# Kernel tuning notes

Hardware: AMD Instinct MI355X
Metric: run time of the kernel (lower is better)

The kernel has to match this reference:

```python
import jax, jax.numpy as jnp
import numpy as np

TEMP = 0.1
LAM = 1.0
NORM_EPS = 1e-12   # torch F.normalize eps
COS_EPS = 1e-8     # torch F.cosine_similarity eps


def l2norm(x, axis):
    n = jnp.sqrt(jnp.sum(x * x, axis=axis, keepdims=True))
    return x / jnp.maximum(n, NORM_EPS)


def cos_sim(a, b, axis):
    na = jnp.sqrt(jnp.sum(a * a, axis=axis))
    nb = jnp.sqrt(jnp.sum(b * b, axis=axis))
    return jnp.sum(a * b, axis=axis) / jnp.maximum(na * nb, COS_EPS)


def setup_inputs() -> dict:
    key = jax.random.key(0)
    k1, k2, k3, k4, k5 = jax.random.split(key, 5)
    B, C, H, W = 32, 256, 32, 32
    return {
        "q_b": jax.random.normal(k1, (B, C, H, W), dtype=jnp.float32),
        "k_b": jax.random.normal(k2, (B, C, H, W), dtype=jnp.float32),
        "q_grid": jax.random.normal(k3, (B, C, H, W), dtype=jnp.float32),
        "k_grid": jax.random.normal(k4, (B, C, H, W), dtype=jnp.float32),
        "labels": jax.random.randint(k5, (B,), 0, 10, dtype=jnp.int64),
    }


def densecl(q_b, k_b, q_grid, k_grid, labels):
    B, C, H, W = q_b.shape
    S = H * W
    q_b = l2norm(q_b, axis=1)
    k_b = l2norm(k_b, axis=1)
    q_grid = l2norm(q_grid, axis=1)
    k_grid = l2norm(k_grid, axis=1)

    q_b_flat = q_b.reshape(B, C, S)
    k_b_flat = k_b.reshape(B, C, S)
    # spatial correspondence: [B, S, S]
    sim = jnp.einsum('bci,bcj->bij', q_b_flat, k_b_flat)
    max_sim_idx = jnp.argmax(sim, axis=-1)  # [B, S]

    Cg = q_grid.shape[1]
    q_grid_flat = q_grid.reshape(B, Cg, S)
    k_grid_flat = k_grid.reshape(B, Cg, S)
    idx = jnp.broadcast_to(max_sim_idx[:, None, :], (B, Cg, S))
    k_matched = jnp.take_along_axis(k_grid_flat, idx, axis=2)
    pos_sim = cos_sim(q_grid_flat, k_matched, axis=1) / TEMP  # [B, S]

    # random negative from a different-label sample (use_prototypes=False path)
    key = jax.random.key(42)
    u = jax.random.uniform(key, (B, B))
    mask = labels[:, None] != labels[None, :]
    neg_idx = jnp.argmax(jnp.where(mask, u, -1.0), axis=1)  # [B]
    neg_k = k_grid_flat[neg_idx]  # [B, Cg, S]
    neg_sim = cos_sim(q_grid_flat, neg_k, axis=1) / TEMP  # [B, S]

    loss = -jnp.log(jnp.exp(pos_sim) / (jnp.exp(pos_sim) + jnp.exp(neg_sim) + 1e-6))
    return jnp.mean(loss)


def reference(q_b, k_b, q_grid, k_grid, labels):
    return densecl(q_b, k_b, q_grid, k_grid, labels) * LAM
```

## Files before the change

kernel.cpp:

```cpp
#include <hip/hip_runtime.h>
#include <hip/hip_bf16.h>
#include <math.h>
#include <stdint.h>

#define BB 32
#define CC 256
#define SS 1024

typedef __attribute__((ext_vector_type(8))) short short8v;
typedef __attribute__((ext_vector_type(4))) float f32x4;

#define ASYNC16(g, l)                                                        \
  __builtin_amdgcn_global_load_lds(                                          \
      (const __attribute__((address_space(1))) void*)(g),                    \
      (__attribute__((address_space(3))) void*)(l), 16, 0, 0)

__device__ __forceinline__ unsigned short bf16_rne(float f) {
  unsigned int u = __float_as_uint(f);
  unsigned int r = (u + 0x7fffu + ((u >> 16) & 1u)) >> 16;
  return (unsigned short)r;
}

__device__ __forceinline__ void tf_round(uint32_t& x0, uint32_t& x1, int r) {
  x0 += x1;
  x1 = (x1 << r) | (x1 >> (32 - r));
  x1 ^= x0;
}

__device__ __forceinline__ void tf_gen(int t, float* u) {
  uint32_t x0 = (uint32_t)t;
  uint32_t x1 = (uint32_t)(t + 512);
  const uint32_t ks0 = 0u, ks1 = 42u, ks2 = 0x1BD11BDAu ^ 0u ^ 42u;
  x0 += ks0; x1 += ks1;
  tf_round(x0, x1, 13); tf_round(x0, x1, 15); tf_round(x0, x1, 26); tf_round(x0, x1, 6);
  x0 += ks1; x1 += ks2 + 1u;
  tf_round(x0, x1, 17); tf_round(x0, x1, 29); tf_round(x0, x1, 16); tf_round(x0, x1, 24);
  x0 += ks2; x1 += ks0 + 2u;
  tf_round(x0, x1, 13); tf_round(x0, x1, 15); tf_round(x0, x1, 26); tf_round(x0, x1, 6);
  x0 += ks0; x1 += ks1 + 3u;
  tf_round(x0, x1, 17); tf_round(x0, x1, 29); tf_round(x0, x1, 16); tf_round(x0, x1, 24);
  x0 += ks1; x1 += ks2 + 4u;
  tf_round(x0, x1, 13); tf_round(x0, x1, 15); tf_round(x0, x1, 26); tf_round(x0, x1, 6);
  x0 += ks2; x1 += ks0 + 5u;
  u[t]       = __uint_as_float((x0 >> 9) | 0x3f800000u) - 1.0f;
  u[t + 512] = __uint_as_float((x1 >> 9) | 0x3f800000u) - 1.0f;
}

__global__ __launch_bounds__(256, 4) void transnorm_kernel(
    const float* __restrict__ qb, const float* __restrict__ kb,
    const float* __restrict__ kg, unsigned short* __restrict__ qt,
    unsigned short* __restrict__ kt, unsigned short* __restrict__ kgt,
    float* __restrict__ invqb, float* __restrict__ invkb,
    float* __restrict__ invkg, const int* __restrict__ labels,
    int* __restrict__ negidx, unsigned long long* __restrict__ best,
    float* __restrict__ out) {
  const int bid = blockIdx.x;
  const int tid = threadIdx.x;

  __shared__ unsigned int tile[64 * 128];
  __shared__ float part[16][65];

  if (bid >= 1536) {
    if (bid == 1536) {
      float* u = (float*)&tile[0];
      tf_gen(tid, u);
      tf_gen(tid + 256, u);
      if (tid == 0) *out = 0.f;
      __syncthreads();
      if (tid < BB) {
        int lb = labels[tid];
        float bestv = -1.0f;
        int bj = 0;
        for (int j = 0; j < BB; ++j) {
          float v = (labels[j] != lb) ? u[tid * BB + j] : -1.0f;
          if (v > bestv) { bestv = v; bj = j; }
        }
        negidx[tid] = bj;
      }
    } else {
      unsigned long long* bp = best + (size_t)(bid - 1537) * 8192 + tid;
#pragma unroll
      for (int i = 0; i < 32; ++i) bp[(size_t)i * 256] = 0ull;
    }
    return;
  }

  const int which = bid >> 9;
  const int sub = bid & 511;
  const int b = sub >> 4;
  const int s0 = (sub & 15) * 64;

  const float* src = (which == 0) ? qb : (which == 1) ? kb : kg;
  unsigned short* dst = (which == 0) ? qt : (which == 1) ? kt : kgt;
  float* inv = (which == 0) ? invqb : (which == 1) ? invkb : invkg;

  const int sg = tid & 15;
  const int cq = tid >> 4;

  const float* sp = src + (size_t)b * CC * SS + s0 + sg * 4;
  float ssq[4] = {0.f, 0.f, 0.f, 0.f};

#pragma unroll
  for (int half = 0; half < 2; ++half) {
    float4 xa[4], xb[4];
#pragma unroll
    for (int kk = 0; kk < 4; ++kk) {
      int cp = cq + 16 * (half * 4 + kk);
      int c = cp * 2;
      xa[kk] = *(const float4*)(sp + ((size_t)c << 10));
      xb[kk] = *(const float4*)(sp + ((size_t)(c + 1) << 10));
    }
#pragma unroll
    for (int kk = 0; kk < 4; ++kk) {
      int cp = cq + 16 * (half * 4 + kk);
      float a[4] = {xa[kk].x, xa[kk].y, xa[kk].z, xa[kk].w};
      float bb[4] = {xb[kk].x, xb[kk].y, xb[kk].z, xb[kk].w};
#pragma unroll
      for (int e = 0; e < 4; ++e) {
        ssq[e] = fmaf(a[e], a[e], ssq[e]);
        ssq[e] = fmaf(bb[e], bb[e], ssq[e]);
        int r = sg * 4 + e;
        int colp = cp ^ (sg << 2);
        tile[r * 128 + colp] =
            (unsigned)bf16_rne(a[e]) | ((unsigned)bf16_rne(bb[e]) << 16);
      }
    }
  }
#pragma unroll
  for (int e = 0; e < 4; ++e) part[cq][sg * 4 + e] = ssq[e];
  __syncthreads();

  const int h = tid >> 5, cw = tid & 31;
  unsigned short* dp = dst + ((size_t)b * SS + s0) * CC;
#pragma unroll
  for (int p = 0; p < 8; ++p) {
    int r = p * 8 + h;
    int colb = (cw * 4) ^ ((r >> 2) << 2);
    uint4 pk = *(const uint4*)&tile[r * 128 + colb];
    *(uint4*)(dp + (size_t)r * CC + cw * 8) = pk;
  }
  if (tid < 64) {
    float s = 0.f;
#pragma unroll
    for (int k = 0; k < 16; ++k) s += part[k][tid];
    inv[b * SS + s0 + tid] = 1.0f / fmaxf(sqrtf(s), 1e-12f);
  }
}

__global__ __launch_bounds__(256, 3) void simargmax_mfma(
    const unsigned short* __restrict__ qt, const unsigned short* __restrict__ kt,
    const float* __restrict__ invk, unsigned long long* __restrict__ best) {
  const int bid0 = blockIdx.x;
  const int W = (bid0 & 7) * 256 + (bid0 >> 3);
  const int b = W >> 6, it = (W >> 3) & 7, jt = W & 7;
  const int t = threadIdx.x, w = t >> 6, l = t & 63;

  __shared__ unsigned short sa[128 * 64];
  __shared__ unsigned short sb[128 * 64];
  __shared__ unsigned long long cand2[128][2];
  __shared__ float sinvk[128];

  if (t < 128) sinvk[t] = invk[b * SS + jt * 128 + t];

  const unsigned short* aG = qt + ((size_t)b * SS + it * 128) * CC;
  const unsigned short* bG = kt + ((size_t)b * SS + jt * 128) * CC;

  f32x4 acc[4][4];
#pragma unroll
  for (int mt = 0; mt < 4; ++mt)
#pragma unroll
    for (int nt = 0; nt < 4; ++nt) acc[mt][nt] = (f32x4){0.f, 0.f, 0.f, 0.f};

  const int r8 = l >> 3, p = l & 7;
  const int q4 = l >> 4, m16 = l & 15;
  const int wi = (w >> 1) * 64, wj = (w & 1) * 64;

  for (int ch = 0; ch < 4; ++ch) {
    __syncthreads();
#pragma unroll
    for (int v = 0; v < 4; ++v) {
      int r = v * 32 + w * 8 + r8;
      int clog = p ^ (r & 7);
      ASYNC16(aG + (size_t)r * CC + ch * 64 + clog * 8, &sa[(v * 32 + w * 8) * 64]);
      ASYNC16(bG + (size_t)r * CC + ch * 64 + clog * 8, &sb[(v * 32 + w * 8) * 64]);
    }
    __syncthreads();
#pragma unroll
    for (int kk = 0; kk < 2; ++kk) {
      short8v af[4], bf[4];
#pragma unroll
      for (int mt = 0; mt < 4; ++mt) {
        int i = wi + mt * 16 + m16;
        int cp = (kk * 4 + q4) ^ (i & 7);
        af[mt] = *(const short8v*)&sa[i * 64 + cp * 8];
        int j = wj + mt * 16 + m16;
        int cq = (kk * 4 + q4) ^ (j & 7);
        bf[mt] = *(const short8v*)&sb[j * 64 + cq * 8];
      }
#pragma unroll
      for (int mt = 0; mt < 4; ++mt)
#pragma unroll
        for (int nt = 0; nt < 4; ++nt)
          acc[mt][nt] = __builtin_amdgcn_mfma_f32_16x16x32_bf16(
              af[mt], bf[nt], acc[mt][nt], 0, 0, 0);
    }
  }

  float siv[4];
#pragma unroll
  for (int nt = 0; nt < 4; ++nt) siv[nt] = sinvk[wj + nt * 16 + m16];

  unsigned long long bp[4][4];
#pragma unroll
  for (int mt = 0; mt < 4; ++mt) {
#pragma unroll
    for (int e = 0; e < 4; ++e) {
      unsigned long long mx = 0ull;
#pragma unroll
      for (int nt = 0; nt < 4; ++nt) {
        float v = acc[mt][nt][e] * siv[nt];
        unsigned int u = __float_as_uint(v);
        u = (u & 0x80000000u) ? ~u : (u | 0x80000000u);
        int col = jt * 128 + wj + nt * 16 + m16;
        unsigned long long pk =
            ((unsigned long long)u << 32) | (unsigned)(1023 - col);
        mx = (pk > mx) ? pk : mx;
      }
      bp[mt][e] = mx;
    }
  }
#pragma unroll
  for (int d = 1; d < 16; d <<= 1) {
#pragma unroll
    for (int mt = 0; mt < 4; ++mt)
#pragma unroll
      for (int e = 0; e < 4; ++e) {
        unsigned long long o = __shfl_xor(bp[mt][e], d, 64);
        if (o > bp[mt][e]) bp[mt][e] = o;
      }
  }
  if (m16 == 0) {
#pragma unroll
    for (int mt = 0; mt < 4; ++mt)
#pragma unroll
      for (int e = 0; e < 4; ++e)
        cand2[wi + mt * 16 + q4 * 4 + e][w & 1] = bp[mt][e];
  }
  __syncthreads();
  if (t < 128) {
    unsigned long long m0 = cand2[t][0], m1 = cand2[t][1];
    atomicMax(&best[b * SS + it * 128 + t], m0 > m1 ? m0 : m1);
  }
}

__global__ void negidx_kernel(const int* __restrict__ labels, int* __restrict__ negidx) {
  __shared__ float u[1024];
  int t = threadIdx.x;
  tf_gen(t, u);
  __syncthreads();
  if (t < BB) {
    int lb = labels[t];
    float bestv = -1.0f;
    int bj = 0;
    for (int j = 0; j < BB; ++j) {
      float v = (labels[j] != lb) ? u[t * BB + j] : -1.0f;
      if (v > bestv) { bestv = v; bj = j; }
    }
    negidx[t] = bj;
  }
}

__global__ __launch_bounds__(256) void loss_fused_kernel(
    const float* __restrict__ qg, const unsigned short* __restrict__ kgt,
    const float* __restrict__ invkg, const unsigned long long* __restrict__ best,
    const int* __restrict__ negidx, float* __restrict__ out) {
  const int tid = threadIdx.x;
  const int s_l = tid & 31, g = tid >> 5;
  const int P0 = blockIdx.x * 32;
  const int b = P0 >> 10;
  const int s = (P0 & (SS - 1)) + s_l;
  const int idx = b * SS + s;
  const int js = 1023 - (int)(best[idx] & 0xffffffffu);
  const int nb = negidx[b];

  const float* qcol = qg + ((size_t)b * CC + g * 32) * SS + s;
  const unsigned short* kp = kgt + ((size_t)b * SS + js) * CC + g * 32;
  const unsigned short* kn = kgt + ((size_t)nb * SS + s) * CC + g * 32;

  float dp = 0.f, dn = 0.f, sq = 0.f;
#pragma unroll
  for (int uu = 0; uu < 4; ++uu) {
    uint4 up = *(const uint4*)(kp + uu * 8);
    uint4 un = *(const uint4*)(kn + uu * 8);
    float q[8];
#pragma unroll
    for (int j = 0; j < 8; ++j) {
      q[j] = qcol[(size_t)(uu * 8 + j) << 10];
      sq = fmaf(q[j], q[j], sq);
    }
    float pv[8], nv[8];
    pv[0] = __uint_as_float(up.x << 16); pv[1] = __uint_as_float(up.x & 0xffff0000u);
    pv[2] = __uint_as_float(up.y << 16); pv[3] = __uint_as_float(up.y & 0xffff0000u);
    pv[4] = __uint_as_float(up.z << 16); pv[5] = __uint_as_float(up.z & 0xffff0000u);
    pv[6] = __uint_as_float(up.w << 16); pv[7] = __uint_as_float(up.w & 0xffff0000u);
    nv[0] = __uint_as_float(un.x << 16); nv[1] = __uint_as_float(un.x & 0xffff0000u);
    nv[2] = __uint_as_float(un.y << 16); nv[3] = __uint_as_float(un.y & 0xffff0000u);
    nv[4] = __uint_as_float(un.z << 16); nv[5] = __uint_as_float(un.z & 0xffff0000u);
    nv[6] = __uint_as_float(un.w << 16); nv[7] = __uint_as_float(un.w & 0xffff0000u);
#pragma unroll
    for (int j = 0; j < 8; ++j) {
      dp = fmaf(q[j], pv[j], dp);
      dn = fmaf(q[j], nv[j], dn);
    }
  }

  __shared__ float rdp[8][33], rdn[8][33], rsq[8][33];
  rdp[g][s_l] = dp;
  rdn[g][s_l] = dn;
  rsq[g][s_l] = sq;
  __syncthreads();
  if (tid < 32) {
    float DP = 0.f, DN = 0.f, SQ = 0.f;
#pragma unroll
    for (int k = 0; k < 8; ++k) {
      DP += rdp[k][tid];
      DN += rdn[k][tid];
      SQ += rsq[k][tid];
    }
    int s2 = (P0 & (SS - 1)) + tid;
    int idx2 = b * SS + s2;
    int js2 = 1023 - (int)(best[idx2] & 0xffffffffu);
    float iq = 1.0f / fmaxf(sqrtf(SQ), 1e-12f);
    float pvv = DP * iq * invkg[b * SS + js2] * 10.0f;
    float nvv = DN * iq * invkg[nb * SS + s2] * 10.0f;
    float elem = logf(expf(pvv) + expf(nvv) + 1e-6f) - pvv;
#pragma unroll
    for (int o = 16; o > 0; o >>= 1) elem += __shfl_down(elem, o, 32);
    if (tid == 0) atomicAdd(out, elem * (1.0f / (BB * SS)));
  }
}

__global__ __launch_bounds__(256) void norms_kernel(
    const float* __restrict__ qb, const float* __restrict__ kb,
    const float* __restrict__ qg, const float* __restrict__ kg,
    float* __restrict__ inv) {
  int t = blockIdx.x * 256 + threadIdx.x;
  int which = t >> 15;
  int bs = t & (BB * SS - 1);
  const float* src = (which == 0) ? qb : (which == 1) ? kb : (which == 2) ? qg : kg;
  int b = bs >> 10;
  int s = bs & (SS - 1);
  const float* p = src + (size_t)b * CC * SS + s;
  float ss = 0.f;
#pragma unroll 8
  for (int c = 0; c < CC; ++c) {
    float x = p[(size_t)c * SS];
    ss = fmaf(x, x, ss);
  }
  float n = fmaxf(sqrtf(ss), 1e-12f);
  inv[t] = 1.0f / n;
}

#define TI 64
#define TJ 128
#define KC 32

__global__ __launch_bounds__(256) void simargmax_kernel(
    const float* __restrict__ qb, const float* __restrict__ kb,
    const float* __restrict__ invq, const float* __restrict__ invk,
    int* __restrict__ amax) {
  const int b = blockIdx.x >> 4;
  const int i0 = (blockIdx.x & 15) * TI;
  const int t = threadIdx.x;
  const int ti = t >> 4;
  const int tj = t & 15;

  __shared__ float aQ[KC][TI];
  __shared__ float bK[KC][TJ];
  __shared__ float redv[TI][16];
  __shared__ int redj[TI][16];

  const float* qbase = qb + (size_t)b * CC * SS + i0;
  const float* kbase = kb + (size_t)b * CC * SS;
  const float* ivq = invq + b * SS + i0;
  const float* ivk = invk + b * SS;

  float best_v = -3.4e38f;
  int best_j = 0;

  for (int j0 = 0; j0 < SS; j0 += TJ) {
    float acc[4][8];
#pragma unroll
    for (int r = 0; r < 4; ++r)
#pragma unroll
      for (int rr = 0; rr < 8; ++rr) acc[r][rr] = 0.f;

    for (int c0 = 0; c0 < CC; c0 += KC) {
      __syncthreads();
#pragma unroll
      for (int v = 0; v < 2; ++v) {
        int f = t + v * 256;
        int cl = f >> 4;
        int sl = (f & 15) << 2;
        float4 qa = *(const float4*)(qbase + (size_t)(c0 + cl) * SS + sl);
        float4 iv = *(const float4*)(ivq + sl);
        aQ[cl][sl + 0] = qa.x * iv.x;
        aQ[cl][sl + 1] = qa.y * iv.y;
        aQ[cl][sl + 2] = qa.z * iv.z;
        aQ[cl][sl + 3] = qa.w * iv.w;
      }
#pragma unroll
      for (int v = 0; v < 4; ++v) {
        int f = t + v * 256;
        int cl = f >> 5;
        int sl = (f & 31) << 2;
        float4 ka = *(const float4*)(kbase + (size_t)(c0 + cl) * SS + j0 + sl);
        float4 ik = *(const float4*)(ivk + j0 + sl);
        bK[cl][sl + 0] = ka.x * ik.x;
        bK[cl][sl + 1] = ka.y * ik.y;
        bK[cl][sl + 2] = ka.z * ik.z;
        bK[cl][sl + 3] = ka.w * ik.w;
      }
      __syncthreads();
#pragma unroll
      for (int kc = 0; kc < KC; ++kc) {
        float4 a0 = *(const float4*)&aQ[kc][ti * 4];
        float4 b0 = *(const float4*)&bK[kc][tj * 8];
        float4 b1 = *(const float4*)&bK[kc][tj * 8 + 4];
        float av[4] = {a0.x, a0.y, a0.z, a0.w};
        float bv[8] = {b0.x, b0.y, b0.z, b0.w, b1.x, b1.y, b1.z, b1.w};
#pragma unroll
        for (int r = 0; r < 4; ++r)
#pragma unroll
          for (int rr = 0; rr < 8; ++rr)
            acc[r][rr] = fmaf(av[r], bv[rr], acc[r][rr]);
      }
    }
    __syncthreads();
#pragma unroll
    for (int r = 0; r < 4; ++r) {
      float v = acc[r][0];
      int jb = j0 + tj * 8;
#pragma unroll
      for (int rr = 1; rr < 8; ++rr) {
        if (acc[r][rr] > v) { v = acc[r][rr]; jb = j0 + tj * 8 + rr; }
      }
      redv[ti * 4 + r][tj] = v;
      redj[ti * 4 + r][tj] = jb;
    }
    __syncthreads();
    if (t < TI) {
#pragma unroll
      for (int ww = 0; ww < 16; ++ww) {
        float v = redv[t][ww];
        if (v > best_v) { best_v = v; best_j = redj[t][ww]; }
      }
    }
  }
  if (t < TI) amax[b * SS + i0 + t] = best_j;
}

__global__ __launch_bounds__(256) void loss_kernel(
    const float* __restrict__ qg, const float* __restrict__ kg,
    const float* __restrict__ invq, const float* __restrict__ invk,
    const int* __restrict__ amax, const int* __restrict__ negidx,
    float* __restrict__ out) {
  int t = blockIdx.x * 256 + threadIdx.x;
  int b = t >> 10;
  int s = t & (SS - 1);
  int js = amax[t];
  int nb = negidx[b];
  const float* qcol = qg + (size_t)b * CC * SS + s;
  const float* kpcol = kg + (size_t)b * CC * SS + js;
  const float* kncol = kg + (size_t)nb * CC * SS + s;
  float dp = 0.f, dn = 0.f;
#pragma unroll 8
  for (int c = 0; c < CC; ++c) {
    float q = qcol[(size_t)c * SS];
    dp = fmaf(q, kpcol[(size_t)c * SS], dp);
    dn = fmaf(q, kncol[(size_t)c * SS], dn);
  }
  float iq = invq[t];
  float pv = dp * iq * invk[b * SS + js] * 10.0f;
  float nv = dn * iq * invk[nb * SS + s] * 10.0f;
  float elem = logf(expf(pv) + expf(nv) + 1e-6f) - pv;

  __shared__ float red[256];
  red[threadIdx.x] = elem;
  __syncthreads();
  for (int o = 128; o > 0; o >>= 1) {
    if (threadIdx.x < o) red[threadIdx.x] += red[threadIdx.x + o];
    __syncthreads();
  }
  if (threadIdx.x == 0) atomicAdd(out, red[0] * (1.0f / (BB * SS)));
}

extern "C" void kernel_launch(void* const* d_in, const int* in_sizes, int n_in,
                              void* d_out, int out_size, void* d_ws, size_t ws_size,
                              hipStream_t stream) {
  const float* qb = (const float*)d_in[0];
  const float* kb = (const float*)d_in[1];
  const float* qg = (const float*)d_in[2];
  const float* kg = (const float*)d_in[3];
  const int* labels = (const int*)d_in[4];

  char* ws = (char*)d_ws;
  float* invqb = (float*)ws;
  float* invkb = (float*)(ws + 128 * 1024);
  float* invkg = (float*)(ws + 256 * 1024);
  unsigned long long* best = (unsigned long long*)(ws + 384 * 1024);
  int* negidx = (int*)(ws + 640 * 1024);
  unsigned short* qt = (unsigned short*)(ws + (1 << 20));
  unsigned short* kt = (unsigned short*)(ws + (17 << 20));
  unsigned short* kgt = (unsigned short*)(ws + (33 << 20));

  const size_t need = (size_t)49 * 1024 * 1024;
  const bool fast = ws_size >= need;

  if (fast) {
    transnorm_kernel<<<1541, 256, 0, stream>>>(qb, kb, kg, qt, kt, kgt, invqb,
                                               invkb, invkg, labels, negidx,
                                               best, (float*)d_out);
    simargmax_mfma<<<2048, 256, 0, stream>>>(qt, kt, invkb, best);
    loss_fused_kernel<<<1024, 256, 0, stream>>>(qg, kgt, invkg, best, negidx,
                                                (float*)d_out);
  } else {
    hipMemsetAsync(d_out, 0, sizeof(float), stream);
    float* inv = (float*)ws;
    int* amax = (int*)(ws + 512 * 1024);
    int* negidx2 = (int*)(ws + 640 * 1024);
    norms_kernel<<<(4 * BB * SS) / 256, 256, 0, stream>>>(qb, kb, qg, kg, inv);
    simargmax_kernel<<<BB * (SS / TI), 256, 0, stream>>>(
        qb, kb, inv + 0 * BB * SS, inv + 1 * BB * SS, amax);
    negidx_kernel<<<1, 512, 0, stream>>>(labels, negidx2);
    loss_kernel<<<(BB * SS) / 256, 256, 0, stream>>>(
        qg, kg, inv + 2 * BB * SS, inv + 3 * BB * SS, amax, negidx2,
        (float*)d_out);
  }
}
```

Measured before the change: 204.7 us.

## Double-buffer LDS tiles in similarity argmax kernel to overlap loads with MFMA

Splits the shared-memory A/B tiles of the similarity/argmax MFMA kernel into two buffers. The async global-to-LDS load of the next K chunk is issued before the MFMA compute on the current chunk, so fetch latency can be hidden behind compute instead of sitting between two barriers. The larger LDS footprint led to lowering the launch-bounds occupancy hint from 3 to 2 blocks per CU, which trades some latency hiding across blocks for this intra-block overlap. The K loop is now fully unrolled into four explicit stages.

```diff
diff --git a/kernel.cpp b/kernel.cpp
--- a/kernel.cpp
+++ b/kernel.cpp
@@ -147,7 +147,43 @@
   }
 }
 
-__global__ __launch_bounds__(256, 3) void simargmax_mfma(
+__device__ __forceinline__ void sim_stage(
+    const unsigned short* __restrict__ aG, const unsigned short* __restrict__ bG,
+    unsigned short* SA, unsigned short* SB, int ch, int w, int r8, int p) {
+#pragma unroll
+  for (int v = 0; v < 4; ++v) {
+    int r = v * 32 + w * 8 + r8;
+    int clog = p ^ (r & 7);
+    ASYNC16(aG + (size_t)r * CC + ch * 64 + clog * 8, &SA[(v * 32 + w * 8) * 64]);
+    ASYNC16(bG + (size_t)r * CC + ch * 64 + clog * 8, &SB[(v * 32 + w * 8) * 64]);
+  }
+}
+
+__device__ __forceinline__ void sim_compute(
+    const unsigned short* SA, const unsigned short* SB, f32x4 acc[4][4],
+    int wi, int wj, int q4, int m16) {
+#pragma unroll
+  for (int kk = 0; kk < 2; ++kk) {
+    short8v af[4], bf[4];
+#pragma unroll
+    for (int mt = 0; mt < 4; ++mt) {
+      int i = wi + mt * 16 + m16;
+      int cp = (kk * 4 + q4) ^ (i & 7);
+      af[mt] = *(const short8v*)&SA[i * 64 + cp * 8];
+      int j = wj + mt * 16 + m16;
+      int cq = (kk * 4 + q4) ^ (j & 7);
+      bf[mt] = *(const short8v*)&SB[j * 64 + cq * 8];
+    }
+#pragma unroll
+    for (int mt = 0; mt < 4; ++mt)
+#pragma unroll
+      for (int nt = 0; nt < 4; ++nt)
+        acc[mt][nt] = __builtin_amdgcn_mfma_f32_16x16x32_bf16(
+            af[mt], bf[nt], acc[mt][nt], 0, 0, 0);
+  }
+}
+
+__global__ __launch_bounds__(256, 2) void simargmax_mfma(
     const unsigned short* __restrict__ qt, const unsigned short* __restrict__ kt,
     const float* __restrict__ invk, unsigned long long* __restrict__ best) {
   const int bid0 = blockIdx.x;
@@ -155,8 +191,10 @@
   const int b = W >> 6, it = (W >> 3) & 7, jt = W & 7;
   const int t = threadIdx.x, w = t >> 6, l = t & 63;
 
-  __shared__ unsigned short sa[128 * 64];
-  __shared__ unsigned short sb[128 * 64];
+  __shared__ unsigned short sa0[128 * 64];
+  __shared__ unsigned short sa1[128 * 64];
+  __shared__ unsigned short sb0[128 * 64];
+  __shared__ unsigned short sb1[128 * 64];
   __shared__ unsigned long long cand2[128][2];
   __shared__ float sinvk[128];
 
@@ -175,36 +213,18 @@
   const int q4 = l >> 4, m16 = l & 15;
   const int wi = (w >> 1) * 64, wj = (w & 1) * 64;
 
-  for (int ch = 0; ch < 4; ++ch) {
-    __syncthreads();
-#pragma unroll
-    for (int v = 0; v < 4; ++v) {
-      int r = v * 32 + w * 8 + r8;
-      int clog = p ^ (r & 7);
-      ASYNC16(aG + (size_t)r * CC + ch * 64 + clog * 8, &sa[(v * 32 + w * 8) * 64]);
-      ASYNC16(bG + (size_t)r * CC + ch * 64 + clog * 8, &sb[(v * 32 + w * 8) * 64]);
-    }
-    __syncthreads();
-#pragma unroll
-    for (int kk = 0; kk < 2; ++kk) {
-      short8v af[4], bf[4];
-#pragma unroll
-      for (int mt = 0; mt < 4; ++mt) {
-        int i = wi + mt * 16 + m16;
-        int cp = (kk * 4 + q4) ^ (i & 7);
-        af[mt] = *(const short8v*)&sa[i * 64 + cp * 8];
-        int j = wj + mt * 16 + m16;
-        int cq = (kk * 4 + q4) ^ (j & 7);
-        bf[mt] = *(const short8v*)&sb[j * 64 + cq * 8];
-      }
-#pragma unroll
-      for (int mt = 0; mt < 4; ++mt)
-#pragma unroll
-        for (int nt = 0; nt < 4; ++nt)
-          acc[mt][nt] = __builtin_amdgcn_mfma_f32_16x16x32_bf16(
-              af[mt], bf[nt], acc[mt][nt], 0, 0, 0);
-    }
-  }
+  sim_stage(aG, bG, sa0, sb0, 0, w, r8, p);
+  __syncthreads();
+  sim_stage(aG, bG, sa1, sb1, 1, w, r8, p);
+  sim_compute(sa0, sb0, acc, wi, wj, q4, m16);
+  __syncthreads();
+  sim_stage(aG, bG, sa0, sb0, 2, w, r8, p);
+  sim_compute(sa1, sb1, acc, wi, wj, q4, m16);
+  __syncthreads();
+  sim_stage(aG, bG, sa1, sb1, 3, w, r8, p);
+  sim_compute(sa0, sb0, acc, wi, wj, q4, m16);
+  __syncthreads();
+  sim_compute(sa1, sb1, acc, wi, wj, q4, m16);
 
   float siv[4];
 #pragma unroll
```

Result: no change. 205.7 us (+0.5%).
